# Optimization experiments

Measured on AMD Instinct MI355X. Metric: run time of the kernel, lower is better.

The kernel has to match this reference:

```python
import jax, jax.numpy as jnp
import numpy as np

N, E = 10000, 160000
IN_C, HID, K = 128, 256, 16


def setup_inputs() -> dict:
    key = jax.random.key(0)
    ks = jax.random.split(key, 8)
    x = jax.random.normal(ks[0], (N, IN_C), jnp.float32)
    edge_index = jax.random.randint(ks[1], (2, E), 0, N, dtype=jnp.int32).astype(jnp.int64)
    edge_attributes = jax.random.uniform(ks[2], (E,), jnp.float32)
    W1 = jax.random.normal(ks[3], (IN_C, HID), jnp.float32) / np.sqrt(IN_C)
    b1 = jnp.zeros((HID,), jnp.float32)
    W2 = jax.random.normal(ks[4], (HID, HID), jnp.float32) / np.sqrt(HID)
    b2 = jnp.zeros((HID,), jnp.float32)
    Wp = jax.random.normal(ks[5], (HID, K), jnp.float32) / np.sqrt(HID)
    bp = jnp.zeros((K,), jnp.float32)
    return dict(x=x, edge_index=edge_index, edge_attributes=edge_attributes,
                W1=W1, b1=b1, W2=W2, b2=b2, Wp=Wp, bp=bp)


def _gcn_conv(x, src, dst, ew, W, b):
    """GCNConv with add_self_loops=True, normalize=True, edge weights."""
    n = x.shape[0]
    loop = jnp.arange(n)
    s = jnp.concatenate([src, loop])
    d = jnp.concatenate([dst, loop])
    w = jnp.concatenate([ew, jnp.ones((n,), x.dtype)])
    deg = jax.ops.segment_sum(w, d, num_segments=n)           # weighted in-degree
    dis = jnp.where(deg > 0, jax.lax.rsqrt(deg), 0.0)         # D^{-1/2}, inf -> 0
    norm = dis[s] * w * dis[d]                                # per-edge coefficient
    h = x @ W                                                 # transform first
    msg = norm[:, None] * h[s]                                # gather from source
    out = jax.ops.segment_sum(msg, d, num_segments=n)         # scatter-add to target
    return out + b


def reference(x, edge_index, edge_attributes, W1, b1, W2, b2, Wp, bp):
    src, dst = edge_index[0], edge_index[1]
    ew = edge_attributes
    h = jax.nn.relu(_gcn_conv(x, src, dst, ew, W1, b1))
    h = jax.nn.relu(_gcn_conv(h, src, dst, ew, W2, b2))

    # to_dense_adj (duplicate edges accumulate)
    adj = jnp.zeros((N, N), h.dtype).at[src, dst].add(ew)

    # DMoNPooling (dropout=0, eval): s = softmax(Linear(h))
    s = jax.nn.softmax(h @ Wp + bp, axis=-1)                  # [N, K]

    out_adj = s.T @ adj @ s                                   # [K, K]
    deg = adj.sum(axis=1)                                     # [N]
    m = deg.sum() / 2
    ca = s.T @ deg[:, None]                                   # [K, 1]
    cb = deg[None, :] @ s                                     # [1, K]
    normalizer = (ca @ cb) / (2 * m)
    spectral_loss = -jnp.trace(out_adj - normalizer) / (2 * m)

    cluster_size = s.sum(axis=0)                              # [K]
    cluster_loss = jnp.linalg.norm(cluster_size) / N * jnp.sqrt(jnp.float32(K)) - 1.0

    loss = 100.0 * (spectral_loss + cluster_loss)
    # PyG returns s with a leading batch dim of 1
    return s[None], loss, 100.0 * spectral_loss, 100.0 * cluster_loss
```

## Files before the change

kernel.cpp:

```cpp
#include <hip/hip_runtime.h>
#include <math.h>


#define ER_BLOCKS 128

typedef unsigned short u16;
typedef __attribute__((ext_vector_type(8))) short short8v;
typedef __attribute__((ext_vector_type(4))) float float4v;
typedef __attribute__((ext_vector_type(4))) unsigned short ushort4v;

__device__ __forceinline__ u16 f2bf_rne(float x) {
  unsigned u = __float_as_uint(x);
  u = (u + 0x7fffu + ((u >> 16) & 1u)) >> 16;
  return (u16)u;
}
__device__ __forceinline__ float bf2f(u16 h) {
  return __uint_as_float(((unsigned)h) << 16);
}

__device__ __forceinline__ bool ei_is_i64(const int* __restrict__ ei) {
  return ((ei[1] | ei[3] | ei[5] | ei[7]) == 0);
}
__device__ __forceinline__ int ld_idx(const int* __restrict__ ei, int pos, bool i64) {
  return i64 ? ei[2 * pos] : ei[pos];
}

__global__ __launch_bounds__(256) void setup_kernel(int4* __restrict__ zp, int zn4,
                                                    const float* __restrict__ x,
                                                    u16* __restrict__ xbf, int nx4,
                                                    const float* __restrict__ W1,
                                                    u16* __restrict__ w1hi, u16* __restrict__ w1lo,
                                                    const float* __restrict__ W2,
                                                    u16* __restrict__ w2hi, u16* __restrict__ w2lo) {
  const int T1 = 256 * 128, T2 = 256 * 256;
  int idx = blockIdx.x * 256 + threadIdx.x;
  if (idx < zn4) {
    zp[idx] = make_int4(0, 0, 0, 0);
    return;
  }
  idx -= zn4;
  if (idx < nx4) {
    float4 v = reinterpret_cast<const float4*>(x)[idx];
    ushort4v o = {f2bf_rne(v.x), f2bf_rne(v.y), f2bf_rne(v.z), f2bf_rne(v.w)};
    reinterpret_cast<ushort4v*>(xbf)[idx] = o;
    return;
  }
  idx -= nx4;
  if (idx < T1) {
    int n = idx >> 7, k = idx & 127;
    float v = W1[k * 256 + n];
    u16 h = f2bf_rne(v);
    w1hi[idx] = h;
    w1lo[idx] = f2bf_rne(v - bf2f(h));
    return;
  }
  idx -= T1;
  if (idx < T2) {
    int n = idx >> 8, k = idx & 255;
    float v = W2[k * 256 + n];
    u16 h = f2bf_rne(v);
    w2hi[idx] = h;
    w2lo[idx] = f2bf_rne(v - bf2f(h));
  }
}

__global__ __launch_bounds__(256) void edge_count(const int* __restrict__ ei,
                                                  const float* __restrict__ ew,
                                                  int* __restrict__ cnt,
                                                  float* __restrict__ deg, int E) {
  int e = blockIdx.x * 256 + threadIdx.x;
  if (e >= E) return;
  bool i64 = ei_is_i64(ei);
  int d = ld_idx(ei, E + e, i64);
  atomicAdd(&cnt[d], 1);
  atomicAdd(&deg[d], ew[e]);
}

__global__ __launch_bounds__(1024) void scan_kernel(const int* __restrict__ cnt,
                                                    int* __restrict__ rowptr, int n) {
  __shared__ int sums[1024];
  int tid = threadIdx.x;
  int CH = (n + 1023) >> 10;
  int beg = tid * CH, end = min(beg + CH, n);
  int s = 0;
  for (int i = beg; i < end; ++i) s += cnt[i];
  sums[tid] = s;
  __syncthreads();
  for (int off = 1; off < 1024; off <<= 1) {
    int v = (tid >= off) ? sums[tid - off] : 0;
    __syncthreads();
    sums[tid] += v;
    __syncthreads();
  }
  int run = (tid == 0) ? 0 : sums[tid - 1];
  for (int i = beg; i < end; ++i) { rowptr[i] = run; run += cnt[i]; }
  if (tid == 1023) rowptr[n] = run;
}

__global__ __launch_bounds__(256) void scatter_edges(const int* __restrict__ ei,
                                                     const float* __restrict__ ew,
                                                     const int* __restrict__ rowptr,
                                                     int* __restrict__ cur,
                                                     const float* __restrict__ deg,
                                                     int* __restrict__ col,
                                                     float* __restrict__ coef, int E) {
  int e = blockIdx.x * 256 + threadIdx.x;
  if (e >= E) return;
  bool i64 = ei_is_i64(ei);
  int s = ld_idx(ei, e, i64);
  int d = ld_idx(ei, E + e, i64);
  int p = rowptr[d] + atomicAdd(&cur[d], 1);
  col[p] = s;
  float ds = 1.0f / sqrtf(deg[s] + 1.0f);
  float dd = 1.0f / sqrtf(deg[d] + 1.0f);
  coef[p] = ds * ew[e] * dd;
}

template <int CH>
__global__ __launch_bounds__(256) void aggregate_pre(const u16* __restrict__ src,
                                                     const int* __restrict__ rowptr,
                                                     const int* __restrict__ col,
                                                     const float* __restrict__ coef,
                                                     const float* __restrict__ deg,
                                                     u16* __restrict__ ohi,
                                                     u16* __restrict__ olo, int N) {
  constexpr int Q = CH / 4;
  constexpr int NS = 256 / Q;
  int i = blockIdx.x;
  int t = threadIdx.x;
  int q = t % Q, slot = t / Q;
  int e0 = rowptr[i], e1 = rowptr[i + 1];
  float4 acc = make_float4(0.f, 0.f, 0.f, 0.f);
  for (int p = e0 + slot; p < e1; p += NS) {
    int c = col[p];
    float w = coef[p];
    ushort4v v = *reinterpret_cast<const ushort4v*>(&src[(size_t)c * CH + q * 4]);
    acc.x += w * bf2f(v[0]); acc.y += w * bf2f(v[1]);
    acc.z += w * bf2f(v[2]); acc.w += w * bf2f(v[3]);
  }
  __shared__ float4 red[256];
  red[t] = acc;
  __syncthreads();
  if (slot == 0) {
#pragma unroll
    for (int s2 = 1; s2 < NS; ++s2) {
      float4 o = red[s2 * Q + q];
      acc.x += o.x; acc.y += o.y; acc.z += o.z; acc.w += o.w;
    }
    float w0 = 1.0f / (deg[i] + 1.0f);
    ushort4v xv = *reinterpret_cast<const ushort4v*>(&src[(size_t)i * CH + q * 4]);
    acc.x += w0 * bf2f(xv[0]); acc.y += w0 * bf2f(xv[1]);
    acc.z += w0 * bf2f(xv[2]); acc.w += w0 * bf2f(xv[3]);
    float a[4] = {acc.x, acc.y, acc.z, acc.w};
    ushort4v hv, lv;
#pragma unroll
    for (int j = 0; j < 4; ++j) {
      u16 h = f2bf_rne(a[j]);
      hv[j] = h;
      lv[j] = f2bf_rne(a[j] - bf2f(h));
    }
    *reinterpret_cast<ushort4v*>(&ohi[(size_t)i * CH + q * 4]) = hv;
    *reinterpret_cast<ushort4v*>(&olo[(size_t)i * CH + q * 4]) = lv;
  }
}

__global__ __launch_bounds__(256) void gemm_mfma(const u16* __restrict__ Ahi,
                                                 const u16* __restrict__ Alo,
                                                 const u16* __restrict__ Wthi,
                                                 const u16* __restrict__ Wtlo,
                                                 const float* __restrict__ bias,
                                                 float* __restrict__ C,
                                                 u16* __restrict__ Cbf,
                                                 int M, int K, int outbf) {
  __shared__ u16 As_hi[64][40], As_lo[64][40];
  __shared__ u16 Bs_hi[64][40], Bs_lo[64][40];
  int tid = threadIdx.x;
  int w = tid >> 6, l = tid & 63;
  int wm = w >> 1, wn = w & 1;
  int row0 = blockIdx.x * 64, col0 = blockIdx.y * 64;
  int srow = tid >> 2, sc = (tid & 3) * 8;
  int fr = l & 15, kg = (l >> 4) * 8;

  float4v acc[2][2];
#pragma unroll
  for (int i = 0; i < 2; ++i)
#pragma unroll
    for (int j = 0; j < 2; ++j) acc[i][j] = (float4v){0.f, 0.f, 0.f, 0.f};

  for (int k0 = 0; k0 < K; k0 += 32) {
    {
      int gr = row0 + srow;
      uint4 zero = make_uint4(0, 0, 0, 0);
      uint4 vh = zero, vl = zero;
      if (gr < M) {
        vh = *reinterpret_cast<const uint4*>(&Ahi[(size_t)gr * K + k0 + sc]);
        vl = *reinterpret_cast<const uint4*>(&Alo[(size_t)gr * K + k0 + sc]);
      }
      *reinterpret_cast<uint4*>(&As_hi[srow][sc]) = vh;
      *reinterpret_cast<uint4*>(&As_lo[srow][sc]) = vl;
      int bn = col0 + srow;
      uint4 bh = *reinterpret_cast<const uint4*>(&Wthi[(size_t)bn * K + k0 + sc]);
      uint4 bl = *reinterpret_cast<const uint4*>(&Wtlo[(size_t)bn * K + k0 + sc]);
      *reinterpret_cast<uint4*>(&Bs_hi[srow][sc]) = bh;
      *reinterpret_cast<uint4*>(&Bs_lo[srow][sc]) = bl;
    }
    __syncthreads();
    short8v ah[2], al[2], bh[2], bl[2];
#pragma unroll
    for (int i = 0; i < 2; ++i) {
      int r = wm * 32 + i * 16 + fr;
      ah[i] = *reinterpret_cast<const short8v*>(&As_hi[r][kg]);
      al[i] = *reinterpret_cast<const short8v*>(&As_lo[r][kg]);
    }
#pragma unroll
    for (int j = 0; j < 2; ++j) {
      int n = wn * 32 + j * 16 + fr;
      bh[j] = *reinterpret_cast<const short8v*>(&Bs_hi[n][kg]);
      bl[j] = *reinterpret_cast<const short8v*>(&Bs_lo[n][kg]);
    }
#pragma unroll
    for (int i = 0; i < 2; ++i)
#pragma unroll
      for (int j = 0; j < 2; ++j) {
        acc[i][j] = __builtin_amdgcn_mfma_f32_16x16x32_bf16(ah[i], bh[j], acc[i][j], 0, 0, 0);
        acc[i][j] = __builtin_amdgcn_mfma_f32_16x16x32_bf16(al[i], bh[j], acc[i][j], 0, 0, 0);
        acc[i][j] = __builtin_amdgcn_mfma_f32_16x16x32_bf16(ah[i], bl[j], acc[i][j], 0, 0, 0);
      }
    __syncthreads();
  }
#pragma unroll
  for (int j = 0; j < 2; ++j) {
    int gc = col0 + wn * 32 + j * 16 + fr;
    float bj = bias[gc];
#pragma unroll
    for (int i = 0; i < 2; ++i) {
#pragma unroll
      for (int r = 0; r < 4; ++r) {
        int gr = row0 + wm * 32 + i * 16 + (l >> 4) * 4 + r;
        if (gr < M) {
          float v = fmaxf(acc[i][j][r] + bj, 0.0f);
          if (outbf) Cbf[(size_t)gr * 256 + gc] = f2bf_rne(v);
          else       C[(size_t)gr * 256 + gc] = v;
        }
      }
    }
  }
}

__global__ __launch_bounds__(256) void pool_kernel(const float* __restrict__ h,
                                                   const float* __restrict__ Wp,
                                                   const float* __restrict__ bp,
                                                   float* __restrict__ s_out,
                                                   float* __restrict__ cs_part, int N) {
  __shared__ float Wps[256 * 16];
  __shared__ float cs_loc[16];
  int tid = threadIdx.x;
  for (int idx = tid; idx < 4096; idx += 256) Wps[idx] = Wp[idx];
  if (tid < 16) cs_loc[tid] = 0.f;
  __syncthreads();
  int lane = tid & 63;
  int wave = tid >> 6;
  int k = lane & 15, g = lane >> 4;
  int node = blockIdx.x * 16 + wave * 4 + g;
  float acc = 0.f;
  if (node < N) {
    const float4* hrow = reinterpret_cast<const float4*>(h + (size_t)node * 256);
#pragma unroll 8
    for (int c4 = 0; c4 < 64; ++c4) {
      float4 hv = hrow[c4];
      int cb = c4 * 4;
      acc += hv.x * Wps[(cb + 0) * 16 + k];
      acc += hv.y * Wps[(cb + 1) * 16 + k];
      acc += hv.z * Wps[(cb + 2) * 16 + k];
      acc += hv.w * Wps[(cb + 3) * 16 + k];
    }
    acc += bp[k];
  }
  float mx = acc;
#pragma unroll
  for (int off = 1; off < 16; off <<= 1) mx = fmaxf(mx, __shfl_xor(mx, off));
  float ex = (node < N) ? expf(acc - mx) : 0.f;
  float sm = ex;
#pragma unroll
  for (int off = 1; off < 16; off <<= 1) sm += __shfl_xor(sm, off);
  float sval = (node < N) ? ex / sm : 0.f;
  if (node < N) s_out[(size_t)node * 16 + k] = sval;
  float v = sval;
  v += __shfl_xor(v, 16);
  v += __shfl_xor(v, 32);
  if (lane < 16) atomicAdd(&cs_loc[lane], v);
  __syncthreads();
  if (tid < 16) cs_part[(size_t)blockIdx.x * 16 + tid] = cs_loc[tid];
}

__global__ __launch_bounds__(256) void edge_reduce(const int* __restrict__ ei,
                                                   const float* __restrict__ ew,
                                                   const float* __restrict__ s,
                                                   float* __restrict__ part,
                                                   const float* __restrict__ cs_part,
                                                   int pool_blocks,
                                                   int* __restrict__ ctr,
                                                   float* __restrict__ out,
                                                   int N, int s_elems, int E) {
  __shared__ float loc[18];
  int tid = threadIdx.x;
  if (tid < 18) loc[tid] = 0.f;
  __syncthreads();
  bool i64 = ei_is_i64(ei);
  float dot = 0.f, w = 0.f;
  float ca[16];
#pragma unroll
  for (int k = 0; k < 16; ++k) ca[k] = 0.f;
  for (int e = blockIdx.x * 256 + tid; e < E; e += gridDim.x * 256) {
    int a = ld_idx(ei, e, i64);
    int b = ld_idx(ei, E + e, i64);
    float we = ew[e];
    const float4* sa = reinterpret_cast<const float4*>(s + (size_t)a * 16);
    const float4* sb = reinterpret_cast<const float4*>(s + (size_t)b * 16);
    float d = 0.f;
#pragma unroll
    for (int q = 0; q < 4; ++q) {
      float4 av = sa[q], bv = sb[q];
      d += av.x * bv.x + av.y * bv.y + av.z * bv.z + av.w * bv.w;
      ca[q * 4 + 0] += we * av.x; ca[q * 4 + 1] += we * av.y;
      ca[q * 4 + 2] += we * av.z; ca[q * 4 + 3] += we * av.w;
    }
    dot += we * d;
    w += we;
  }
#pragma unroll
  for (int off = 32; off; off >>= 1) {
    dot += __shfl_xor(dot, off);
    w += __shfl_xor(w, off);
#pragma unroll
    for (int k = 0; k < 16; ++k) ca[k] += __shfl_xor(ca[k], off);
  }
  if ((tid & 63) == 0) {
    atomicAdd(&loc[0], dot);
    atomicAdd(&loc[1], w);
#pragma unroll
    for (int k = 0; k < 16; ++k) atomicAdd(&loc[2 + k], ca[k]);
  }
  __syncthreads();
  if (tid < 18) part[(size_t)blockIdx.x * 18 + tid] = loc[tid];

  __shared__ bool amLast;
  __threadfence();
  if (tid == 0) amLast = (atomicAdd(ctr, 1) == (int)gridDim.x - 1);
  __syncthreads();
  if (!amLast) return;

  __shared__ float red[18];
  __shared__ float csl[256];
  __shared__ float cs[16];
  if (tid < 18) {
    float a = 0.f;
    for (int b = 0; b < (int)gridDim.x; ++b) a += part[(size_t)b * 18 + tid];
    red[tid] = a;
  }
  {
    int k = tid & 15, sl = tid >> 4;
    float a = 0.f;
    for (int b = sl; b < pool_blocks; b += 16) a += cs_part[(size_t)b * 16 + k];
    csl[tid] = a;
  }
  __syncthreads();
  if (tid < 16) {
    float a = 0.f;
#pragma unroll
    for (int sl = 0; sl < 16; ++sl) a += csl[sl * 16 + tid];
    cs[tid] = a;
  }
  __syncthreads();
  if (tid == 0) {
    float tr = red[0], m2 = red[1];
    float ca2 = 0.f, cs2 = 0.f;
    for (int k = 0; k < 16; ++k) {
      ca2 += red[2 + k] * red[2 + k];
      cs2 += cs[k] * cs[k];
    }
    float sp = -(tr - ca2 / m2) / m2;
    float cl = sqrtf(cs2) / (float)N * 4.0f - 1.0f;
    out[s_elems + 0] = 100.f * (sp + cl);
    out[s_elems + 1] = 100.f * sp;
    out[s_elems + 2] = 100.f * cl;
  }
}

extern "C" void kernel_launch(void* const* d_in, const int* in_sizes, int n_in,
                              void* d_out, int out_size, void* d_ws, size_t ws_size,
                              hipStream_t stream) {
  const float* x  = (const float*)d_in[0];
  const int*   ei = (const int*)d_in[1];
  const float* ew = (const float*)d_in[2];
  const float* W1 = (const float*)d_in[3];
  const float* b1 = (const float*)d_in[4];
  const float* W2 = (const float*)d_in[5];
  const float* b2 = (const float*)d_in[6];
  const float* Wp = (const float*)d_in[7];
  const float* bp = (const float*)d_in[8];
  float* out = (float*)d_out;

  const int IN_C = 128, HID = 256;
  const int N = in_sizes[0] / IN_C;
  const int E = in_sizes[2];
  const int pool_blocks = (N + 15) / 16;

  char* p = (char*)d_ws;
  auto alloc = [&](size_t b) { char* r = p; p += (b + 255) & ~(size_t)255; return r; };
  float* deg     = (float*)alloc((size_t)N * 4);
  int*   cnt     = (int*)alloc((size_t)N * 4);
  int*   cur     = (int*)alloc((size_t)N * 4);
  int*   ctr     = (int*)alloc(256);
  char*  zero_end = p;
  u16*   xbf     = (u16*)alloc((size_t)N * IN_C * 2);
  u16*   hbf     = (u16*)alloc((size_t)N * HID * 2);
  u16*   axhi    = (u16*)alloc((size_t)N * IN_C * 2);
  u16*   axlo    = (u16*)alloc((size_t)N * IN_C * 2);
  u16*   ahhi    = (u16*)alloc((size_t)N * HID * 2);
  u16*   ahlo    = (u16*)alloc((size_t)N * HID * 2);
  float* h2      = (float*)alloc((size_t)N * HID * 4);
  u16*   w1hi    = (u16*)alloc((size_t)256 * 128 * 2);
  u16*   w1lo    = (u16*)alloc((size_t)256 * 128 * 2);
  u16*   w2hi    = (u16*)alloc((size_t)256 * 256 * 2);
  u16*   w2lo    = (u16*)alloc((size_t)256 * 256 * 2);
  int*   rowptr  = (int*)alloc((size_t)(N + 1) * 4);
  int*   col     = (int*)alloc((size_t)E * 4);
  float* coef    = (float*)alloc((size_t)E * 4);
  float* epart   = (float*)alloc((size_t)ER_BLOCKS * 18 * 4);
  float* cs_part = (float*)alloc((size_t)pool_blocks * 16 * 4);
  if ((size_t)(p - (char*)d_ws) > ws_size) return;

  int zn4 = (int)((zero_end - (char*)deg) >> 4);
  int nx4 = (N * IN_C) / 4;
  int setup_items = zn4 + nx4 + 256 * 128 + 256 * 256;
  setup_kernel<<<(setup_items + 255) / 256, 256, 0, stream>>>(
      (int4*)deg, zn4, x, xbf, nx4, W1, w1hi, w1lo, W2, w2hi, w2lo);

  int eb = (E + 255) / 256;
  edge_count<<<eb, 256, 0, stream>>>(ei, ew, cnt, deg, E);
  scan_kernel<<<1, 1024, 0, stream>>>(cnt, rowptr, N);
  scatter_edges<<<eb, 256, 0, stream>>>(ei, ew, rowptr, cur, deg, col, coef, E);

  dim3 gg((N + 63) / 64, HID / 64);
  aggregate_pre<128><<<N, 256, 0, stream>>>(xbf, rowptr, col, coef, deg, axhi, axlo, N);
  gemm_mfma<<<gg, 256, 0, stream>>>(axhi, axlo, w1hi, w1lo, b1, nullptr, hbf, N, IN_C, 1);
  aggregate_pre<256><<<N, 256, 0, stream>>>(hbf, rowptr, col, coef, deg, ahhi, ahlo, N);
  gemm_mfma<<<gg, 256, 0, stream>>>(ahhi, ahlo, w2hi, w2lo, b2, h2, nullptr, N, HID, 0);

  pool_kernel<<<pool_blocks, 256, 0, stream>>>(h2, Wp, bp, out, cs_part, N);
  edge_reduce<<<ER_BLOCKS, 256, 0, stream>>>(ei, ew, out, epart, cs_part, pool_blocks,
                                             ctr, out, N, N * 16, E);
}
```

Baseline: 174.3 us.

## Precompute weighted out-degree, slim edge reduce, widen aggregate vector loads

Source-side weighted degree is now accumulated in edge_count, which lets the per-cluster degree sums (s^T deg) be computed in the pooling kernel instead of per edge. edge_reduce now only computes the weighted s_a·s_b dot product, using 4 lanes per edge and more blocks, and a separate finalize kernel replaces the last-block counter pattern. aggregate_pre switches to 8-wide bf16 loads per thread. This adds one atomic per edge and one extra kernel launch in exchange for lighter edge-reduce register pressure and better parallelism.

Result: faster. 144.4 us (-17.2%).

```diff
diff --git a/kernel.cpp b/kernel.cpp
--- a/kernel.cpp
+++ b/kernel.cpp
@@ -2,12 +2,13 @@
 #include <math.h>
 
 
-#define ER_BLOCKS 128
+#define ER_BLOCKS 512
 
 typedef unsigned short u16;
 typedef __attribute__((ext_vector_type(8))) short short8v;
 typedef __attribute__((ext_vector_type(4))) float float4v;
 typedef __attribute__((ext_vector_type(4))) unsigned short ushort4v;
+typedef __attribute__((ext_vector_type(8))) unsigned short ushort8v;
 
 __device__ __forceinline__ u16 f2bf_rne(float x) {
   unsigned u = __float_as_uint(x);
@@ -67,13 +68,17 @@
 __global__ __launch_bounds__(256) void edge_count(const int* __restrict__ ei,
                                                   const float* __restrict__ ew,
                                                   int* __restrict__ cnt,
-                                                  float* __restrict__ deg, int E) {
+                                                  float* __restrict__ deg,
+                                                  float* __restrict__ wdeg, int E) {
   int e = blockIdx.x * 256 + threadIdx.x;
   if (e >= E) return;
   bool i64 = ei_is_i64(ei);
+  int s = ld_idx(ei, e, i64);
   int d = ld_idx(ei, E + e, i64);
+  float we = ew[e];
   atomicAdd(&cnt[d], 1);
-  atomicAdd(&deg[d], ew[e]);
+  atomicAdd(&deg[d], we);
+  atomicAdd(&wdeg[s], we);
 }
 
 __global__ __launch_bounds__(1024) void scan_kernel(const int* __restrict__ cnt,
@@ -124,43 +129,41 @@
                                                      const float* __restrict__ deg,
                                                      u16* __restrict__ ohi,
                                                      u16* __restrict__ olo, int N) {
-  constexpr int Q = CH / 4;
+  constexpr int Q = CH / 8;
   constexpr int NS = 256 / Q;
   int i = blockIdx.x;
   int t = threadIdx.x;
   int q = t % Q, slot = t / Q;
   int e0 = rowptr[i], e1 = rowptr[i + 1];
-  float4 acc = make_float4(0.f, 0.f, 0.f, 0.f);
+  float a[8] = {};
   for (int p = e0 + slot; p < e1; p += NS) {
     int c = col[p];
     float w = coef[p];
-    ushort4v v = *reinterpret_cast<const ushort4v*>(&src[(size_t)c * CH + q * 4]);
-    acc.x += w * bf2f(v[0]); acc.y += w * bf2f(v[1]);
-    acc.z += w * bf2f(v[2]); acc.w += w * bf2f(v[3]);
-  }
-  __shared__ float4 red[256];
-  red[t] = acc;
+    ushort8v v = *reinterpret_cast<const ushort8v*>(&src[(size_t)c * CH + q * 8]);
+#pragma unroll
+    for (int j = 0; j < 8; ++j) a[j] += w * bf2f(v[j]);
+  }
+  __shared__ float red[256][9];
+#pragma unroll
+  for (int j = 0; j < 8; ++j) red[t][j] = a[j];
   __syncthreads();
   if (slot == 0) {
 #pragma unroll
-    for (int s2 = 1; s2 < NS; ++s2) {
-      float4 o = red[s2 * Q + q];
-      acc.x += o.x; acc.y += o.y; acc.z += o.z; acc.w += o.w;
-    }
+    for (int s2 = 1; s2 < NS; ++s2)
+#pragma unroll
+      for (int j = 0; j < 8; ++j) a[j] += red[s2 * Q + q][j];
     float w0 = 1.0f / (deg[i] + 1.0f);
-    ushort4v xv = *reinterpret_cast<const ushort4v*>(&src[(size_t)i * CH + q * 4]);
-    acc.x += w0 * bf2f(xv[0]); acc.y += w0 * bf2f(xv[1]);
-    acc.z += w0 * bf2f(xv[2]); acc.w += w0 * bf2f(xv[3]);
-    float a[4] = {acc.x, acc.y, acc.z, acc.w};
-    ushort4v hv, lv;
-#pragma unroll
-    for (int j = 0; j < 4; ++j) {
+    ushort8v xv = *reinterpret_cast<const ushort8v*>(&src[(size_t)i * CH + q * 8]);
+    ushort8v hv, lv;
+#pragma unroll
+    for (int j = 0; j < 8; ++j) {
+      a[j] += w0 * bf2f(xv[j]);
       u16 h = f2bf_rne(a[j]);
       hv[j] = h;
       lv[j] = f2bf_rne(a[j] - bf2f(h));
     }
-    *reinterpret_cast<ushort4v*>(&ohi[(size_t)i * CH + q * 4]) = hv;
-    *reinterpret_cast<ushort4v*>(&olo[(size_t)i * CH + q * 4]) = lv;
+    *reinterpret_cast<ushort8v*>(&ohi[(size_t)i * CH + q * 8]) = hv;
+    *reinterpret_cast<ushort8v*>(&olo[(size_t)i * CH + q * 8]) = lv;
   }
 }
 
@@ -250,20 +253,22 @@
 __global__ __launch_bounds__(256) void pool_kernel(const float* __restrict__ h,
                                                    const float* __restrict__ Wp,
                                                    const float* __restrict__ bp,
+                                                   const float* __restrict__ wdeg,
                                                    float* __restrict__ s_out,
-                                                   float* __restrict__ cs_part, int N) {
+                                                   float* __restrict__ pp, int N) {
   __shared__ float Wps[256 * 16];
-  __shared__ float cs_loc[16];
+  __shared__ float loc[33];
   int tid = threadIdx.x;
   for (int idx = tid; idx < 4096; idx += 256) Wps[idx] = Wp[idx];
-  if (tid < 16) cs_loc[tid] = 0.f;
+  if (tid < 33) loc[tid] = 0.f;
   __syncthreads();
   int lane = tid & 63;
   int wave = tid >> 6;
   int k = lane & 15, g = lane >> 4;
   int node = blockIdx.x * 16 + wave * 4 + g;
-  float acc = 0.f;
+  float acc = 0.f, wd = 0.f;
   if (node < N) {
+    wd = wdeg[node];
     const float4* hrow = reinterpret_cast<const float4*>(h + (size_t)node * 256);
 #pragma unroll 8
     for (int c4 = 0; c4 < 64; ++c4) {
@@ -286,98 +291,93 @@
   float sval = (node < N) ? ex / sm : 0.f;
   if (node < N) s_out[(size_t)node * 16 + k] = sval;
   float v = sval;
-  v += __shfl_xor(v, 16);
-  v += __shfl_xor(v, 32);
-  if (lane < 16) atomicAdd(&cs_loc[lane], v);
-  __syncthreads();
-  if (tid < 16) cs_part[(size_t)blockIdx.x * 16 + tid] = cs_loc[tid];
+  float v2 = wd * sval;
+  float v3 = (k == 0) ? wd : 0.f;
+  v += __shfl_xor(v, 16);  v += __shfl_xor(v, 32);
+  v2 += __shfl_xor(v2, 16); v2 += __shfl_xor(v2, 32);
+  v3 += __shfl_xor(v3, 16); v3 += __shfl_xor(v3, 32);
+  if (lane < 16) {
+    atomicAdd(&loc[lane], v);
+    atomicAdd(&loc[16 + lane], v2);
+  }
+  if (lane == 0) atomicAdd(&loc[32], v3);
+  __syncthreads();
+  if (tid < 33) pp[(size_t)blockIdx.x * 33 + tid] = loc[tid];
 }
 
 __global__ __launch_bounds__(256) void edge_reduce(const int* __restrict__ ei,
                                                    const float* __restrict__ ew,
                                                    const float* __restrict__ s,
-                                                   float* __restrict__ part,
-                                                   const float* __restrict__ cs_part,
-                                                   int pool_blocks,
-                                                   int* __restrict__ ctr,
-                                                   float* __restrict__ out,
-                                                   int N, int s_elems, int E) {
-  __shared__ float loc[18];
+                                                   float* __restrict__ part, int E) {
   int tid = threadIdx.x;
-  if (tid < 18) loc[tid] = 0.f;
-  __syncthreads();
   bool i64 = ei_is_i64(ei);
-  float dot = 0.f, w = 0.f;
-  float ca[16];
-#pragma unroll
-  for (int k = 0; k < 16; ++k) ca[k] = 0.f;
-  for (int e = blockIdx.x * 256 + tid; e < E; e += gridDim.x * 256) {
+  int le = tid >> 2, sub = tid & 3;
+  int epi = gridDim.x * 64;
+  float acc = 0.f;
+  for (int e = blockIdx.x * 64 + le; e < E; e += epi) {
     int a = ld_idx(ei, e, i64);
     int b = ld_idx(ei, E + e, i64);
-    float we = ew[e];
-    const float4* sa = reinterpret_cast<const float4*>(s + (size_t)a * 16);
-    const float4* sb = reinterpret_cast<const float4*>(s + (size_t)b * 16);
-    float d = 0.f;
-#pragma unroll
-    for (int q = 0; q < 4; ++q) {
-      float4 av = sa[q], bv = sb[q];
-      d += av.x * bv.x + av.y * bv.y + av.z * bv.z + av.w * bv.w;
-      ca[q * 4 + 0] += we * av.x; ca[q * 4 + 1] += we * av.y;
-      ca[q * 4 + 2] += we * av.z; ca[q * 4 + 3] += we * av.w;
-    }
-    dot += we * d;
-    w += we;
-  }
-#pragma unroll
-  for (int off = 32; off; off >>= 1) {
-    dot += __shfl_xor(dot, off);
-    w += __shfl_xor(w, off);
-#pragma unroll
-    for (int k = 0; k < 16; ++k) ca[k] += __shfl_xor(ca[k], off);
-  }
+    float w = ew[e];
+    float4 av = *reinterpret_cast<const float4*>(s + (size_t)a * 16 + sub * 4);
+    float4 bv = *reinterpret_cast<const float4*>(s + (size_t)b * 16 + sub * 4);
+    float d = av.x * bv.x + av.y * bv.y + av.z * bv.z + av.w * bv.w;
+    d += __shfl_xor(d, 1);
+    d += __shfl_xor(d, 2);
+    acc += w * d;
+  }
+#pragma unroll
+  for (int off = 4; off < 64; off <<= 1) acc += __shfl_xor(acc, off);
+  __shared__ float loc;
+  if (tid == 0) loc = 0.f;
+  __syncthreads();
+  if ((tid & 63) == 0) atomicAdd(&loc, acc);
+  __syncthreads();
+  if (tid == 0) part[blockIdx.x] = loc;
+}
+
+__global__ __launch_bounds__(256) void finalize(const float* __restrict__ epart,
+                                                const float* __restrict__ pp, int pb,
+                                                float* __restrict__ out,
+                                                int N, int s_elems) {
+  __shared__ float cred[256];
+  __shared__ float vals[32];
+  __shared__ float scal[2];
+  int tid = threadIdx.x;
+  float a = 0.f;
+  for (int b = tid; b < ER_BLOCKS; b += 256) a += epart[b];
+  float wv = 0.f;
+  for (int b = tid; b < pb; b += 256) wv += pp[(size_t)b * 33 + 32];
+#pragma unroll
+  for (int off = 1; off < 64; off <<= 1) {
+    a += __shfl_xor(a, off);
+    wv += __shfl_xor(wv, off);
+  }
+  if (tid == 0) { scal[0] = 0.f; scal[1] = 0.f; }
+  __syncthreads();
   if ((tid & 63) == 0) {
-    atomicAdd(&loc[0], dot);
-    atomicAdd(&loc[1], w);
-#pragma unroll
-    for (int k = 0; k < 16; ++k) atomicAdd(&loc[2 + k], ca[k]);
-  }
-  __syncthreads();
-  if (tid < 18) part[(size_t)blockIdx.x * 18 + tid] = loc[tid];
-
-  __shared__ bool amLast;
-  __threadfence();
-  if (tid == 0) amLast = (atomicAdd(ctr, 1) == (int)gridDim.x - 1);
-  __syncthreads();
-  if (!amLast) return;
-
-  __shared__ float red[18];
-  __shared__ float csl[256];
-  __shared__ float cs[16];
-  if (tid < 18) {
-    float a = 0.f;
-    for (int b = 0; b < (int)gridDim.x; ++b) a += part[(size_t)b * 18 + tid];
-    red[tid] = a;
+    atomicAdd(&scal[0], a);
+    atomicAdd(&scal[1], wv);
   }
   {
-    int k = tid & 15, sl = tid >> 4;
-    float a = 0.f;
-    for (int b = sl; b < pool_blocks; b += 16) a += cs_part[(size_t)b * 16 + k];
-    csl[tid] = a;
-  }
-  __syncthreads();
-  if (tid < 16) {
-    float a = 0.f;
-#pragma unroll
-    for (int sl = 0; sl < 16; ++sl) a += csl[sl * 16 + tid];
-    cs[tid] = a;
+    int k = tid & 31, sl = tid >> 5;
+    float c = 0.f;
+    for (int b = sl; b < pb; b += 8) c += pp[(size_t)b * 33 + k];
+    cred[tid] = c;
+  }
+  __syncthreads();
+  if (tid < 32) {
+    float c = cred[tid];
+#pragma unroll
+    for (int sl = 1; sl < 8; ++sl) c += cred[sl * 32 + tid];
+    vals[tid] = c;
   }
   __syncthreads();
   if (tid == 0) {
-    float tr = red[0], m2 = red[1];
+    float tr = scal[0], m2 = scal[1];
     float ca2 = 0.f, cs2 = 0.f;
     for (int k = 0; k < 16; ++k) {
-      ca2 += red[2 + k] * red[2 + k];
-      cs2 += cs[k] * cs[k];
+      cs2 += vals[k] * vals[k];
+      ca2 += vals[16 + k] * vals[16 + k];
     }
     float sp = -(tr - ca2 / m2) / m2;
     float cl = sqrtf(cs2) / (float)N * 4.0f - 1.0f;
@@ -409,9 +409,9 @@
   char* p = (char*)d_ws;
   auto alloc = [&](size_t b) { char* r = p; p += (b + 255) & ~(size_t)255; return r; };
   float* deg     = (float*)alloc((size_t)N * 4);
+  float* wdeg    = (float*)alloc((size_t)N * 4);
   int*   cnt     = (int*)alloc((size_t)N * 4);
   int*   cur     = (int*)alloc((size_t)N * 4);
-  int*   ctr     = (int*)alloc(256);
   char*  zero_end = p;
   u16*   xbf     = (u16*)alloc((size_t)N * IN_C * 2);
   u16*   hbf     = (u16*)alloc((size_t)N * HID * 2);
@@ -427,8 +427,8 @@
   int*   rowptr  = (int*)alloc((size_t)(N + 1) * 4);
   int*   col     = (int*)alloc((size_t)E * 4);
   float* coef    = (float*)alloc((size_t)E * 4);
-  float* epart   = (float*)alloc((size_t)ER_BLOCKS * 18 * 4);
-  float* cs_part = (float*)alloc((size_t)pool_blocks * 16 * 4);
+  float* epart   = (float*)alloc((size_t)ER_BLOCKS * 4);
+  float* pp      = (float*)alloc((size_t)pool_blocks * 33 * 4);
   if ((size_t)(p - (char*)d_ws) > ws_size) return;
 
   int zn4 = (int)((zero_end - (char*)deg) >> 4);
@@ -438,7 +438,7 @@
       (int4*)deg, zn4, x, xbf, nx4, W1, w1hi, w1lo, W2, w2hi, w2lo);
 
   int eb = (E + 255) / 256;
-  edge_count<<<eb, 256, 0, stream>>>(ei, ew, cnt, deg, E);
+  edge_count<<<eb, 256, 0, stream>>>(ei, ew, cnt, deg, wdeg, E);
   scan_kernel<<<1, 1024, 0, stream>>>(cnt, rowptr, N);
   scatter_edges<<<eb, 256, 0, stream>>>(ei, ew, rowptr, cur, deg, col, coef, E);
 
@@ -448,7 +448,7 @@
   aggregate_pre<256><<<N, 256, 0, stream>>>(hbf, rowptr, col, coef, deg, ahhi, ahlo, N);
   gemm_mfma<<<gg, 256, 0, stream>>>(ahhi, ahlo, w2hi, w2lo, b2, h2, nullptr, N, HID, 0);
 
-  pool_kernel<<<pool_blocks, 256, 0, stream>>>(h2, Wp, bp, out, cs_part, N);
-  edge_reduce<<<ER_BLOCKS, 256, 0, stream>>>(ei, ew, out, epart, cs_part, pool_blocks,
-                                             ctr, out, N, N * 16, E);
-}
+  pool_kernel<<<pool_blocks, 256, 0, stream>>>(h2, Wp, bp, wdeg, out, pp, N);
+  edge_reduce<<<ER_BLOCKS, 256, 0, stream>>>(ei, ew, out, epart, E);
+  finalize<<<1, 256, 0, stream>>>(epart, pp, pool_blocks, out, N, N * 16);
+}
```
